# Performance work log

Hardware: AMD Instinct MI355X
Metric: run time of the kernel (lower is better)

The kernel has to match this reference:

```python
import jax, jax.numpy as jnp
import numpy as np

NORM_S = 3.0  # normalize_scale, learn_scale=False
NUM_CLASSES = 32


def setup_inputs() -> dict:
    key = jax.random.key(0)
    k1, k2 = jax.random.split(key)
    x = jax.random.normal(k1, (512, 128), dtype=jnp.float32)
    labels = jax.random.randint(k2, (512,), 0, NUM_CLASSES, dtype=jnp.int64)
    return {"x": x, "labels": labels}


def reference(x, labels):
    # L2-normalize rows and scale (MyTripletLoss.forward)
    f = NORM_S * x / jnp.linalg.norm(x, axis=1, keepdims=True)
    # pairwise squared distances, clamped at 0 (pairwise_distances)
    sq = jnp.sum(f * f, axis=1)
    D = jnp.clip(sq[:, None] + sq[None, :] - 2.0 * (f @ f.T), 0.0, None)  # [N,N]
    N = x.shape[0]
    # triplet_type == 0: valid triplet (i,j,k) iff i!=j, l_i==l_j, l_i!=l_k
    same = (labels[:, None] == labels[None, :]) & (~jnp.eye(N, dtype=bool))  # [i,j]
    diff = labels[:, None] != labels[None, :]                                # [i,k]
    mask = same[:, :, None] & diff[:, None, :]                               # [i,j,k]
    # DBL loss: log(1 + exp(D_ij - D_ik)) = softplus
    lt = jax.nn.softplus(D[:, :, None] - D[:, None, :])                      # [i,j,k]
    triplet_count = jnp.sum(mask).astype(lt.dtype)
    loss = jnp.sum(jnp.where(mask, lt, 0.0)) / triplet_count
    return loss.reshape(1)
```

## Files before the change

### kernel.cpp

```cpp
#include <hip/hip_runtime.h>
#include <math.h>

#define N 512
#define DIM 128
#define TT 32
#define PADS 132
#define NTRI (16 * 17 / 2)


__global__ void __launch_bounds__(256) gram_kernel(const float* __restrict__ x,
                                                   float* __restrict__ D) {
    __shared__ float xi[TT * PADS];
    __shared__ float xj[TT * PADS];
    __shared__ float rnA[TT];
    __shared__ float rnB[TT];

    int t = threadIdx.x;

    int b = blockIdx.x;
    int bi = (int)((sqrtf(8.0f * (float)b + 1.0f) - 1.0f) * 0.5f);
    while ((bi + 1) * (bi + 2) / 2 <= b) ++bi;
    while (bi * (bi + 1) / 2 > b) --bi;
    int bj = b - bi * (bi + 1) / 2;

    const float4* srcA = (const float4*)(x + bi * TT * DIM);
    const float4* srcB = (const float4*)(x + bj * TT * DIM);
    #pragma unroll
    for (int k = 0; k < (TT * DIM / 4) / 256; ++k) {
        int e = t + k * 256;
        int r = e >> 5, c4 = e & 31;
        *((float4*)(xi + r * PADS + 4 * c4)) = srcA[e];
        *((float4*)(xj + r * PADS + 4 * c4)) = srcB[e];
    }
    __syncthreads();

    {
        int quart = t & 3, r = t >> 2;
        const float* base = (r < TT) ? (xi + r * PADS) : (xj + (r - TT) * PADS);
        const float4* a = (const float4*)(base + quart * 32);
        float s0 = 0.0f, s1 = 0.0f;
        #pragma unroll
        for (int q = 0; q < 8; q += 2) {
            float4 a0 = a[q], a1 = a[q + 1];
            s0 += a0.x * a0.x + a0.y * a0.y + a0.z * a0.z + a0.w * a0.w;
            s1 += a1.x * a1.x + a1.y * a1.y + a1.z * a1.z + a1.w * a1.w;
        }
        float ss = s0 + s1;
        ss += __shfl_xor(ss, 1, 64);
        ss += __shfl_xor(ss, 2, 64);
        if (quart == 0) {
            if (r < TT) rnA[r] = rsqrtf(ss);
            else        rnB[r - TT] = rsqrtf(ss);
        }
    }
    __syncthreads();

    int tx = t & 15, ty = t >> 4;
    int i0 = ty, i1 = ty + 16, j0 = tx, j1 = tx + 16;
    float acc00 = 0.0f, acc01 = 0.0f, acc10 = 0.0f, acc11 = 0.0f;
    const float4* A0 = (const float4*)(xi + i0 * PADS);
    const float4* A1 = (const float4*)(xi + i1 * PADS);
    const float4* B0 = (const float4*)(xj + j0 * PADS);
    const float4* B1 = (const float4*)(xj + j1 * PADS);
    #pragma unroll 8
    for (int k4 = 0; k4 < DIM / 4; ++k4) {
        float4 a0 = A0[k4], a1 = A1[k4], b0 = B0[k4], b1 = B1[k4];
        acc00 += a0.x * b0.x + a0.y * b0.y + a0.z * b0.z + a0.w * b0.w;
        acc01 += a0.x * b1.x + a0.y * b1.y + a0.z * b1.z + a0.w * b1.w;
        acc10 += a1.x * b0.x + a1.y * b0.y + a1.z * b0.z + a1.w * b0.w;
        acc11 += a1.x * b1.x + a1.y * b1.y + a1.z * b1.z + a1.w * b1.w;
    }
    float ri0 = rnA[i0], ri1 = rnA[i1], rj0 = rnB[j0], rj1 = rnB[j1];
    float t00 = 18.0f * fmaxf(0.0f, 1.0f - acc00 * ri0 * rj0);
    float t01 = 18.0f * fmaxf(0.0f, 1.0f - acc01 * ri0 * rj1);
    float t10 = 18.0f * fmaxf(0.0f, 1.0f - acc10 * ri1 * rj0);
    float t11 = 18.0f * fmaxf(0.0f, 1.0f - acc11 * ri1 * rj1);

    {
        int gi0 = bi * TT + i0, gi1 = bi * TT + i1;
        int gj0 = bj * TT + j0, gj1 = bj * TT + j1;
        D[gi0 * N + gj0] = t00;
        D[gi0 * N + gj1] = t01;
        D[gi1 * N + gj0] = t10;
        D[gi1 * N + gj1] = t11;
    }

    if (bi != bj) {
        __syncthreads();
        float* Tt = xi;
        Tt[j0 * 33 + i0] = t00;
        Tt[j1 * 33 + i0] = t01;
        Tt[j0 * 33 + i1] = t10;
        Tt[j1 * 33 + i1] = t11;
        __syncthreads();
        float m00 = Tt[i0 * 33 + j0], m01 = Tt[i0 * 33 + j1];
        float m10 = Tt[i1 * 33 + j0], m11 = Tt[i1 * 33 + j1];
        int ga0 = bj * TT + i0, ga1 = bj * TT + i1;
        int gb0 = bi * TT + j0, gb1 = bi * TT + j1;
        D[ga0 * N + gb0] = m00;
        D[ga0 * N + gb1] = m01;
        D[ga1 * N + gb0] = m10;
        D[ga1 * N + gb1] = m11;
    }
}

__global__ void __launch_bounds__(256) loss_kernel(const float* __restrict__ Dm,
                                                   const int* __restrict__ labels,
                                                   float* __restrict__ sums,
                                                   float* __restrict__ cnts) {
    __shared__ int   lab[N];
    __shared__ float sameD[N];
    __shared__ float diffD[N];
    __shared__ float esame[N];
    __shared__ int   cS[8], cD[8];
    __shared__ float red[4];

    int i = blockIdx.x, t = threadIdx.x;
    lab[t]       = labels[t];
    lab[t + 256] = labels[t + 256];
    float d0 = Dm[i * N + t];
    float d1 = Dm[i * N + t + 256];
    __syncthreads();

    int li = lab[i];
    int lane = t & 63, w = t >> 6;
    bool pS0 = (lab[t] == li) && (t != i);
    bool pD0 = (lab[t] != li);
    bool pS1 = (lab[t + 256] == li) && ((t + 256) != i);
    bool pD1 = (lab[t + 256] != li);
    unsigned long long bS0 = __ballot(pS0);
    unsigned long long bD0 = __ballot(pD0);
    unsigned long long bS1 = __ballot(pS1);
    unsigned long long bD1 = __ballot(pD1);
    if (lane == 0) {
        cS[w]     = __popcll(bS0); cD[w]     = __popcll(bD0);
        cS[w + 4] = __popcll(bS1); cD[w + 4] = __popcll(bD1);
    }
    __syncthreads();
    int baseS0 = 0, baseD0 = 0, baseS1 = 0, baseD1 = 0, ns = 0, nd = 0;
    #pragma unroll
    for (int s = 0; s < 8; ++s) {
        int cs = cS[s], cd = cD[s];
        if (s < w)     { baseS0 += cs; baseD0 += cd; }
        if (s < w + 4) { baseS1 += cs; baseD1 += cd; }
        ns += cs; nd += cd;
    }
    unsigned long long lt = (1ull << lane) - 1ull;
    if (pS0) sameD[baseS0 + __popcll(bS0 & lt)] = d0;
    if (pD0) diffD[baseD0 + __popcll(bD0 & lt)] = d0;
    if (pS1) sameD[baseS1 + __popcll(bS1 & lt)] = d1;
    if (pD1) diffD[baseD1 + __popcll(bD1 & lt)] = d1;
    __syncthreads();

    if (t < ns)       esame[t]       = __expf(sameD[t]);
    if (t + 256 < ns) esame[t + 256] = __expf(sameD[t + 256]);
    __syncthreads();

    float ek0 = (t < nd)       ? __expf(-diffD[t])       : 0.0f;
    float ek1 = (t + 256 < nd) ? __expf(-diffD[t + 256]) : 0.0f;
    float lsum = 0.0f;
    for (int js = 0; js < ns; ++js) {
        float es = esame[js];
        lsum += __log2f(fmaf(es, ek0, 1.0f)) + __log2f(fmaf(es, ek1, 1.0f));
    }
    lsum *= 0.6931471805599453f;

    #pragma unroll
    for (int off = 32; off > 0; off >>= 1) lsum += __shfl_xor(lsum, off, 64);
    if ((t & 63) == 0) red[t >> 6] = lsum;
    __syncthreads();
    if (t == 0) {
        sums[i] = red[0] + red[1] + red[2] + red[3];
        cnts[i] = (float)(ns * nd);
    }
}

__global__ void __launch_bounds__(256) finalize_kernel(const float* __restrict__ sums,
                                                       const float* __restrict__ cnts,
                                                       float* __restrict__ out) {
    __shared__ float2 red[256];
    int t = threadIdx.x;
    float2 v;
    v.x = sums[t] + sums[t + 256];
    v.y = cnts[t] + cnts[t + 256];
    red[t] = v;
    __syncthreads();
    #pragma unroll
    for (int s = 128; s > 0; s >>= 1) {
        if (t < s) {
            red[t].x += red[t + s].x;
            red[t].y += red[t + s].y;
        }
        __syncthreads();
    }
    if (t == 0) out[0] = red[0].x / red[0].y;
}

extern "C" void kernel_launch(void* const* d_in, const int* in_sizes, int n_in,
                              void* d_out, int out_size, void* d_ws, size_t ws_size,
                              hipStream_t stream) {
    const float* x      = (const float*)d_in[0];
    const int*   labels = (const int*)d_in[1];
    float*       out    = (float*)d_out;

    float* Dm   = (float*)d_ws;
    float* sums = Dm + N * N;
    float* cnts = sums + N;

    gram_kernel<<<NTRI, 256, 0, stream>>>(x, Dm);
    loss_kernel<<<N, 256, 0, stream>>>(Dm, labels, sums, cnts);
    finalize_kernel<<<1, 256, 0, stream>>>(sums, cnts, out);
}
```

Baseline: 63.28 us.

## Fuse distance-row computation into loss kernel and drop the Gram kernel

```diff
diff --git a/kernel.cpp b/kernel.cpp
--- a/kernel.cpp
+++ b/kernel.cpp
@@ -3,126 +3,98 @@
 
 #define N 512
 #define DIM 128
-#define TT 32
-#define PADS 132
-#define NTRI (16 * 17 / 2)
+#define ROWS 64
+#define PASSES (N / ROWS)
+#define TW 132
 
 
-__global__ void __launch_bounds__(256) gram_kernel(const float* __restrict__ x,
-                                                   float* __restrict__ D) {
-    __shared__ float xi[TT * PADS];
-    __shared__ float xj[TT * PADS];
-    __shared__ float rnA[TT];
-    __shared__ float rnB[TT];
-
-    int t = threadIdx.x;
-
-    int b = blockIdx.x;
-    int bi = (int)((sqrtf(8.0f * (float)b + 1.0f) - 1.0f) * 0.5f);
-    while ((bi + 1) * (bi + 2) / 2 <= b) ++bi;
-    while (bi * (bi + 1) / 2 > b) --bi;
-    int bj = b - bi * (bi + 1) / 2;
-
-    const float4* srcA = (const float4*)(x + bi * TT * DIM);
-    const float4* srcB = (const float4*)(x + bj * TT * DIM);
-    #pragma unroll
-    for (int k = 0; k < (TT * DIM / 4) / 256; ++k) {
-        int e = t + k * 256;
-        int r = e >> 5, c4 = e & 31;
-        *((float4*)(xi + r * PADS + 4 * c4)) = srcA[e];
-        *((float4*)(xj + r * PADS + 4 * c4)) = srcB[e];
-    }
-    __syncthreads();
-
-    {
-        int quart = t & 3, r = t >> 2;
-        const float* base = (r < TT) ? (xi + r * PADS) : (xj + (r - TT) * PADS);
-        const float4* a = (const float4*)(base + quart * 32);
-        float s0 = 0.0f, s1 = 0.0f;
-        #pragma unroll
-        for (int q = 0; q < 8; q += 2) {
-            float4 a0 = a[q], a1 = a[q + 1];
-            s0 += a0.x * a0.x + a0.y * a0.y + a0.z * a0.z + a0.w * a0.w;
-            s1 += a1.x * a1.x + a1.y * a1.y + a1.z * a1.z + a1.w * a1.w;
-        }
-        float ss = s0 + s1;
-        ss += __shfl_xor(ss, 1, 64);
-        ss += __shfl_xor(ss, 2, 64);
-        if (quart == 0) {
-            if (r < TT) rnA[r] = rsqrtf(ss);
-            else        rnB[r - TT] = rsqrtf(ss);
-        }
-    }
-    __syncthreads();
-
-    int tx = t & 15, ty = t >> 4;
-    int i0 = ty, i1 = ty + 16, j0 = tx, j1 = tx + 16;
-    float acc00 = 0.0f, acc01 = 0.0f, acc10 = 0.0f, acc11 = 0.0f;
-    const float4* A0 = (const float4*)(xi + i0 * PADS);
-    const float4* A1 = (const float4*)(xi + i1 * PADS);
-    const float4* B0 = (const float4*)(xj + j0 * PADS);
-    const float4* B1 = (const float4*)(xj + j1 * PADS);
-    #pragma unroll 8
-    for (int k4 = 0; k4 < DIM / 4; ++k4) {
-        float4 a0 = A0[k4], a1 = A1[k4], b0 = B0[k4], b1 = B1[k4];
-        acc00 += a0.x * b0.x + a0.y * b0.y + a0.z * b0.z + a0.w * b0.w;
-        acc01 += a0.x * b1.x + a0.y * b1.y + a0.z * b1.z + a0.w * b1.w;
-        acc10 += a1.x * b0.x + a1.y * b0.y + a1.z * b0.z + a1.w * b0.w;
-        acc11 += a1.x * b1.x + a1.y * b1.y + a1.z * b1.z + a1.w * b1.w;
-    }
-    float ri0 = rnA[i0], ri1 = rnA[i1], rj0 = rnB[j0], rj1 = rnB[j1];
-    float t00 = 18.0f * fmaxf(0.0f, 1.0f - acc00 * ri0 * rj0);
-    float t01 = 18.0f * fmaxf(0.0f, 1.0f - acc01 * ri0 * rj1);
-    float t10 = 18.0f * fmaxf(0.0f, 1.0f - acc10 * ri1 * rj0);
-    float t11 = 18.0f * fmaxf(0.0f, 1.0f - acc11 * ri1 * rj1);
-
-    {
-        int gi0 = bi * TT + i0, gi1 = bi * TT + i1;
-        int gj0 = bj * TT + j0, gj1 = bj * TT + j1;
-        D[gi0 * N + gj0] = t00;
-        D[gi0 * N + gj1] = t01;
-        D[gi1 * N + gj0] = t10;
-        D[gi1 * N + gj1] = t11;
-    }
-
-    if (bi != bj) {
-        __syncthreads();
-        float* Tt = xi;
-        Tt[j0 * 33 + i0] = t00;
-        Tt[j1 * 33 + i0] = t01;
-        Tt[j0 * 33 + i1] = t10;
-        Tt[j1 * 33 + i1] = t11;
-        __syncthreads();
-        float m00 = Tt[i0 * 33 + j0], m01 = Tt[i0 * 33 + j1];
-        float m10 = Tt[i1 * 33 + j0], m11 = Tt[i1 * 33 + j1];
-        int ga0 = bj * TT + i0, ga1 = bj * TT + i1;
-        int gb0 = bi * TT + j0, gb1 = bi * TT + j1;
-        D[ga0 * N + gb0] = m00;
-        D[ga0 * N + gb1] = m01;
-        D[ga1 * N + gb0] = m10;
-        D[ga1 * N + gb1] = m11;
-    }
-}
-
-__global__ void __launch_bounds__(256) loss_kernel(const float* __restrict__ Dm,
-                                                   const int* __restrict__ labels,
-                                                   float* __restrict__ sums,
-                                                   float* __restrict__ cnts) {
+__global__ void __launch_bounds__(256) fused_kernel(const float* __restrict__ x,
+                                                    const int* __restrict__ labels,
+                                                    float* __restrict__ sums,
+                                                    float* __restrict__ cnts) {
+    __shared__ float tile[ROWS * TW];
+    __shared__ float xrow[DIM];
+    __shared__ float rnB[ROWS];
     __shared__ int   lab[N];
     __shared__ float sameD[N];
     __shared__ float diffD[N];
     __shared__ float esame[N];
     __shared__ int   cS[8], cD[8];
     __shared__ float red[4];
+    __shared__ float rni_sh;
 
     int i = blockIdx.x, t = threadIdx.x;
+
     lab[t]       = labels[t];
     lab[t + 256] = labels[t + 256];
-    float d0 = Dm[i * N + t];
-    float d1 = Dm[i * N + t + 256];
+
+    if (t < 32) {
+        float4 v = ((const float4*)(x + i * DIM))[t];
+        ((float4*)xrow)[t] = v;
+        float s = v.x * v.x + v.y * v.y + v.z * v.z + v.w * v.w;
+        s += __shfl_xor(s, 1, 64);
+        s += __shfl_xor(s, 2, 64);
+        s += __shfl_xor(s, 4, 64);
+        s += __shfl_xor(s, 8, 64);
+        s += __shfl_xor(s, 16, 64);
+        if (t == 0) rni_sh = rsqrtf(s);
+    }
     __syncthreads();
+    float rni = rni_sh;
+    int li = lab[i];
 
-    int li = lab[i];
+    int myw = t >> 6;
+    int jl  = t & 63;
+    float d0 = 0.0f, d1 = 0.0f;
+
+    float4 pre[8];
+    {
+        const float4* src = (const float4*)x;
+        #pragma unroll
+        for (int k = 0; k < 8; ++k) pre[k] = src[t + 256 * k];
+    }
+
+    for (int p = 0; p < PASSES; ++p) {
+        #pragma unroll
+        for (int k = 0; k < 8; ++k) {
+            int e = t + 256 * k;
+            int r = e >> 5, c4 = e & 31;
+            float4 v = pre[k];
+            *((float4*)(tile + r * TW + 4 * c4)) = v;
+            float s = v.x * v.x + v.y * v.y + v.z * v.z + v.w * v.w;
+            s += __shfl_xor(s, 1, 64);
+            s += __shfl_xor(s, 2, 64);
+            s += __shfl_xor(s, 4, 64);
+            s += __shfl_xor(s, 8, 64);
+            s += __shfl_xor(s, 16, 64);
+            if ((t & 31) == 0) rnB[r] = rsqrtf(s);
+        }
+        __syncthreads();
+
+        if (p < PASSES - 1) {
+            const float4* src = (const float4*)(x + (p + 1) * ROWS * DIM);
+            #pragma unroll
+            for (int k = 0; k < 8; ++k) pre[k] = src[t + 256 * k];
+        }
+
+        bool act0 = (p == myw);
+        bool act1 = (p == 4 + myw);
+        if (act0 || act1) {
+            const float4* B = (const float4*)(tile + jl * TW);
+            const float4* A = (const float4*)xrow;
+            float acc = 0.0f;
+            #pragma unroll 8
+            for (int k4 = 0; k4 < DIM / 4; ++k4) {
+                float4 a = A[k4], b = B[k4];
+                acc += a.x * b.x + a.y * b.y + a.z * b.z + a.w * b.w;
+            }
+            float dv = 18.0f * fmaxf(0.0f, 1.0f - acc * rni * rnB[jl]);
+            if (act0) d0 = dv;
+            else      d1 = dv;
+        }
+        __syncthreads();
+    }
+
     int lane = t & 63, w = t >> 6;
     bool pS0 = (lab[t] == li) && (t != i);
     bool pD0 = (lab[t] != li);
@@ -175,25 +147,22 @@
     }
 }
 
-__global__ void __launch_bounds__(256) finalize_kernel(const float* __restrict__ sums,
-                                                       const float* __restrict__ cnts,
-                                                       float* __restrict__ out) {
-    __shared__ float2 red[256];
+__global__ void __launch_bounds__(64) finalize_kernel(const float* __restrict__ sums,
+                                                      const float* __restrict__ cnts,
+                                                      float* __restrict__ out) {
     int t = threadIdx.x;
-    float2 v;
-    v.x = sums[t] + sums[t + 256];
-    v.y = cnts[t] + cnts[t + 256];
-    red[t] = v;
-    __syncthreads();
+    const float4* S = (const float4*)sums;
+    const float4* C = (const float4*)cnts;
+    float4 s0 = S[t], s1 = S[t + 64];
+    float4 c0 = C[t], c1 = C[t + 64];
+    float s = s0.x + s0.y + s0.z + s0.w + s1.x + s1.y + s1.z + s1.w;
+    float c = c0.x + c0.y + c0.z + c0.w + c1.x + c1.y + c1.z + c1.w;
     #pragma unroll
-    for (int s = 128; s > 0; s >>= 1) {
-        if (t < s) {
-            red[t].x += red[t + s].x;
-            red[t].y += red[t + s].y;
-        }
-        __syncthreads();
+    for (int off = 32; off > 0; off >>= 1) {
+        s += __shfl_xor(s, off, 64);
+        c += __shfl_xor(c, off, 64);
     }
-    if (t == 0) out[0] = red[0].x / red[0].y;
+    if (t == 0) out[0] = s / c;
 }
 
 extern "C" void kernel_launch(void* const* d_in, const int* in_sizes, int n_in,
@@ -203,11 +172,9 @@
     const int*   labels = (const int*)d_in[1];
     float*       out    = (float*)d_out;
 
-    float* Dm   = (float*)d_ws;
-    float* sums = Dm + N * N;
+    float* sums = (float*)d_ws;
     float* cnts = sums + N;
 
-    gram_kernel<<<NTRI, 256, 0, stream>>>(x, Dm);
-    loss_kernel<<<N, 256, 0, stream>>>(Dm, labels, sums, cnts);
-    finalize_kernel<<<1, 256, 0, stream>>>(sums, cnts, out);
+    fused_kernel<<<N, 256, 0, stream>>>(x, labels, sums, cnts);
+    finalize_kernel<<<1, 64, 0, stream>>>(sums, cnts, out);
 }
```

After: 82.20 us. 1.3x slower.
